# Performance work log

Measured on AMD Instinct MI355X. Metric: run time of the kernel, lower is better.

Reference implementation:

```python
import jax, jax.numpy as jnp
import numpy as np

B, N, F, FS, OUT, S, H, K = 1024, 256, 64, 128, 128, 4, 4, 4
EPS = 1e-5   # BatchNorm1d eps
BIG = 1e9    # sentinel distance for invalid nodes

# fully-connected segment edges (S nodes per graph, B graphs, flat node indexing)
_base = np.array([(i, j) for i in range(S) for j in range(S) if i != j], dtype=np.int32).T
_offs = (np.arange(B, dtype=np.int32) * S)[:, None]
CSRC = jnp.asarray((_base[0][None, :] + _offs).reshape(-1))
CDST = jnp.asarray((_base[1][None, :] + _offs).reshape(-1))
CMASK = jnp.ones(CSRC.shape[0], jnp.float32)


def _bn_relu(h, gamma, beta):
    # BatchNorm1d in training mode: biased batch statistics over the node axis
    mu = h.mean(0)
    var = jnp.var(h, axis=0)
    return jax.nn.relu((h - mu) * jax.lax.rsqrt(var + EPS) * gamma + beta)


def _graph_conv(x, src, dst, emask, W, b, gamma, beta):
    # linear -> gather(src) -> scatter-add(dst) -> degree norm -> BN -> ReLU
    h = x @ W + b
    agg = jax.ops.segment_sum(h[src] * emask[:, None], dst, num_segments=x.shape[0])
    deg = jnp.clip(jax.ops.segment_sum(emask, dst, num_segments=x.shape[0]), 1.0, None)
    return _bn_relu(h + agg / deg[:, None], gamma, beta)


def _knn_edges(positions, presence):
    # edges (i -> j) for each valid node i to its K nearest valid neighbors j
    valid = presence > 0.5                                    # [B,N]
    n_valid = valid.sum(-1)                                   # [B]
    diff = positions[:, :, None, :] - positions[:, None, :, :]
    d2 = jax.lax.stop_gradient(jnp.sum(diff * diff, -1))      # squared dist, same ordering as cdist
    d2 = jnp.where(valid[:, None, :], d2, BIG)                # mask invalid columns
    negv, idx = jax.lax.top_k(-d2, K + 1)                     # nearest first; idx[...,0] is self (dist 0)
    nbr, nd = idx[:, :, 1:], -negv[:, :, 1:]                  # [B,N,K]
    emask = valid[:, :, None] & (n_valid[:, None, None] >= 2) & (nd < 0.5 * BIG)
    offs = (jnp.arange(B) * N)[:, None, None]
    src = jnp.broadcast_to(jnp.arange(N)[None, :, None] + offs, (B, N, K)).reshape(-1)
    dst = jnp.where(emask, nbr + offs, 0).reshape(-1)
    return src, dst, emask.reshape(-1).astype(jnp.float32)


def setup_inputs() -> dict:
    key = jax.random.key(0)
    ks = jax.random.split(key, 16)
    rn = lambda k, shp, s=0.05: jax.random.normal(k, shp, jnp.float32) * s
    return {
        "axle_features": jax.random.normal(ks[0], (B, N, F), jnp.float32),
        "axle_positions": jax.random.normal(ks[1], (B, N, 2), jnp.float32),
        "presence_scores": jax.random.uniform(ks[2], (B, N), jnp.float32),
        "seg_queries": jax.random.normal(ks[3], (S, F), jnp.float32),
        "wq": rn(ks[4], (F, F)), "bq": jnp.zeros((F,), jnp.float32),
        "wk": rn(ks[5], (F, F)), "bk": jnp.zeros((F,), jnp.float32),
        "w_a2s": rn(ks[6], (F, FS)), "b_a2s": jnp.zeros((FS,), jnp.float32),
        "w_s2a": rn(ks[7], (FS, F)), "b_s2a": jnp.zeros((F,), jnp.float32),
        "coarse_W": rn(ks[8], (2, FS, FS)), "coarse_b": jnp.zeros((2, FS), jnp.float32),
        "coarse_gamma": jnp.ones((2, FS), jnp.float32), "coarse_beta": jnp.zeros((2, FS), jnp.float32),
        "fine_W": rn(ks[9], (3, F, F)), "fine_b": jnp.zeros((3, F), jnp.float32),
        "fine_gamma": jnp.ones((3, F), jnp.float32), "fine_beta": jnp.zeros((3, F), jnp.float32),
        "w_out": rn(ks[10], (F, OUT)), "b_out": jnp.zeros((OUT,), jnp.float32),
    }


def reference(axle_features, axle_positions, presence_scores, seg_queries, wq, bq, wk, bk,
              w_a2s, b_a2s, w_s2a, b_s2a, coarse_W, coarse_b, coarse_gamma, coarse_beta,
              fine_W, fine_b, fine_gamma, fine_beta, w_out, b_out):
    hd = F // H
    # LearnableSegmentation: MHA attention weights (head-averaged), then softmax over segments
    q = (seg_queries @ wq + bq).reshape(S, H, hd)
    k = (axle_features @ wk + bk).reshape(B, N, H, hd)
    scores = jnp.einsum('shd,bnhd->bhsn', q, k) / np.sqrt(hd)
    attn = jax.nn.softmax(scores, -1).mean(1)                 # [B,S,N]
    assign = jax.nn.softmax(jnp.swapaxes(attn, 1, 2), -1)     # [B,N,S]
    # segment pooling + coarse GNN over fully-connected segment graph
    proj = axle_features @ w_a2s + b_a2s                      # [B,N,FS]
    sf = jnp.einsum('bns,bnf->bsf', assign, proj).reshape(B * S, FS)
    for l in range(coarse_W.shape[0]):
        sf = _graph_conv(sf, CSRC, CDST, CMASK, coarse_W[l], coarse_b[l], coarse_gamma[l], coarse_beta[l])
    ctx = jnp.einsum('bns,bsf->bnf', assign, sf.reshape(B, S, FS)) @ w_s2a + b_s2a
    # fine GNN over kNN axle graph
    src, dst, em = _knn_edges(axle_positions, presence_scores)
    af = (axle_features + ctx).reshape(B * N, F)
    for l in range(fine_W.shape[0]):
        af = _graph_conv(af, src, dst, em, fine_W[l], fine_b[l], fine_gamma[l], fine_beta[l])
    # presence-weighted pooling + output projection
    pw = presence_scores[:, :, None]
    g = (af.reshape(B, N, F) * pw).sum(1) / jnp.clip(pw.sum(1), 1e-8, None)
    return g @ w_out + b_out
```

## Files before the change

kernel.cpp:

```cpp
#include <hip/hip_runtime.h>
#include <hip/hip_bf16.h>
#include <math.h>

#define BB   1024
#define NN   256
#define FF   64
#define FSS  128
#define OUTT 128
#define SS   4
#define HH   4
#define KK   4
#define HDD  16
#define EPSF 1e-5f
#define BIGF 1000000000.0f
#define ROWB 72
#define ROWA 68

typedef __attribute__((ext_vector_type(8))) short short8;
typedef __attribute__((ext_vector_type(4))) float f32x4;

static __device__ __forceinline__ unsigned short f2bf(float f) {
  union { float f; unsigned u; } x; x.f = f;
  unsigned u = x.u + 0x7fffu + ((x.u >> 16) & 1u);
  return (unsigned short)(u >> 16);
}
static __device__ __forceinline__ float bf2f(unsigned short h) {
  union { unsigned u; float f; } x; x.u = ((unsigned)h) << 16;
  return x.f;
}
static __device__ __forceinline__ float bflo(unsigned u) {
  union { unsigned u; float f; } x; x.u = u << 16; return x.f;
}
static __device__ __forceinline__ float bfhi(unsigned u) {
  union { unsigned u; float f; } x; x.u = u & 0xffff0000u; return x.f;
}
static __device__ __forceinline__ unsigned pack2(float a, float b) {
  return (unsigned)f2bf(a) | ((unsigned)f2bf(b) << 16);
}

__global__ __launch_bounds__(256) void k_prep(
    const float* __restrict__ sq, const float* __restrict__ wq, const float* __restrict__ bq,
    const float* __restrict__ wk, const float* __restrict__ bk,
    float* __restrict__ V_o, float* __restrict__ c_o)
{
  const int tid = threadIdx.x;
  __shared__ float sq_s[SS*FF];
  __shared__ float q_s[SS*FF];
  sq_s[tid] = sq[tid];
  __syncthreads();
  {
    int s = tid >> 6, f = tid & 63;
    float acc = bq[f];
    for (int c = 0; c < FF; ++c) acc += sq_s[s*FF+c] * wq[c*FF+f];
    q_s[s*FF+f] = acc;
  }
  __syncthreads();
  {
    int c = tid & 63, jb = (tid >> 6) * 4;
    for (int jj = 0; jj < 4; ++jj) {
      int j = jb + jj, h = j >> 2, s = j & 3;
      float acc = 0.f;
      for (int d = 0; d < HDD; ++d)
        acc += wk[c*FF + h*HDD + d] * q_s[s*FF + h*HDD + d];
      V_o[c*16 + j] = acc * 0.25f;
    }
  }
  if (tid < 16) {
    int h = tid >> 2, s = tid & 3;
    float acc = 0.f;
    for (int d = 0; d < HDD; ++d) acc += bk[h*HDD+d] * q_s[s*FF + h*HDD + d];
    c_o[tid] = acc * 0.25f;
  }
}

__global__ __launch_bounds__(256, 3) void k_attn_sf(
    const float* __restrict__ axle,
    const float* __restrict__ Vm, const float* __restrict__ cv,
    const float* __restrict__ w_a2s, const float* __restrict__ b_a2s,
    float* __restrict__ assign_o, float* __restrict__ sf_o)
{
  const int b = blockIdx.x, tid = threadIdx.x;
  const int wv = tid >> 6, ln = tid & 63;
  __shared__ __align__(16) unsigned short xb_a[NN*ROWA];
  __shared__ __align__(16) unsigned char u_buf[16*NN*2];
  __shared__ float mz_s[16][2];
  __hip_bfloat16* sc_s = (__hip_bfloat16*)u_buf;
  float (*as_s)[SS]    = (float (*)[SS])u_buf;
  float* t_s           = (float*)(u_buf + 4096);
  float* As_s          = (float*)(u_buf + 4096 + 1024);

  const float* afb = axle + (size_t)b*NN*FF;
  const float4* in4 = reinterpret_cast<const float4*>(afb);
  for (int i4 = tid; i4 < NN*FF/4; i4 += 256) {
    float4 v = in4[i4];
    int n = i4 >> 4, c4 = (i4 & 15) * 4;
    uint2 pk; pk.x = pack2(v.x, v.y); pk.y = pack2(v.z, v.w);
    *reinterpret_cast<uint2*>(&xb_a[n*ROWA + c4]) = pk;
  }
  __syncthreads();

  {
    float sc[16];
    #pragma unroll
    for (int j = 0; j < 16; ++j) sc[j] = cv[j];
    #pragma unroll
    for (int k = 0; k < 16; ++k) {
      uint2 pk = *reinterpret_cast<const uint2*>(&xb_a[tid*ROWA + 4*k]);
      float x0 = bflo(pk.x), x1 = bfhi(pk.x), x2 = bflo(pk.y), x3 = bfhi(pk.y);
      #pragma unroll
      for (int j = 0; j < 16; ++j) {
        float a = fmaf(x0, Vm[(4*k+0)*16+j], sc[j]);
        a = fmaf(x1, Vm[(4*k+1)*16+j], a);
        a = fmaf(x2, Vm[(4*k+2)*16+j], a);
        sc[j] = fmaf(x3, Vm[(4*k+3)*16+j], a);
      }
    }
    #pragma unroll
    for (int j = 0; j < 16; ++j) sc_s[j*NN + tid] = __float2bfloat16(sc[j]);
  }
  __syncthreads();

  for (int r = 0; r < 4; ++r) {
    int row = wv*4 + r;
    float v0 = __bfloat162float(sc_s[row*NN + ln]);
    float v1 = __bfloat162float(sc_s[row*NN + ln + 64]);
    float v2 = __bfloat162float(sc_s[row*NN + ln + 128]);
    float v3 = __bfloat162float(sc_s[row*NN + ln + 192]);
    float m = fmaxf(fmaxf(v0,v1), fmaxf(v2,v3));
    #pragma unroll
    for (int o = 32; o; o >>= 1) m = fmaxf(m, __shfl_xor(m, o));
    float z = __expf(v0-m) + __expf(v1-m) + __expf(v2-m) + __expf(v3-m);
    #pragma unroll
    for (int o = 32; o; o >>= 1) z += __shfl_xor(z, o);
    if (ln == 0) { mz_s[row][0] = m; mz_s[row][1] = 1.f/z; }
  }
  __syncthreads();

  float4 av;
  {
    float at0 = 0.f, at1 = 0.f, at2 = 0.f, at3 = 0.f;
    #pragma unroll
    for (int h = 0; h < HH; ++h) {
      at0 += __expf(__bfloat162float(sc_s[(h*4+0)*NN + tid]) - mz_s[h*4+0][0]) * mz_s[h*4+0][1];
      at1 += __expf(__bfloat162float(sc_s[(h*4+1)*NN + tid]) - mz_s[h*4+1][0]) * mz_s[h*4+1][1];
      at2 += __expf(__bfloat162float(sc_s[(h*4+2)*NN + tid]) - mz_s[h*4+2][0]) * mz_s[h*4+2][1];
      at3 += __expf(__bfloat162float(sc_s[(h*4+3)*NN + tid]) - mz_s[h*4+3][0]) * mz_s[h*4+3][1];
    }
    at0 *= 0.25f; at1 *= 0.25f; at2 *= 0.25f; at3 *= 0.25f;
    float m = fmaxf(fmaxf(at0,at1), fmaxf(at2,at3));
    float e0=__expf(at0-m), e1=__expf(at1-m), e2=__expf(at2-m), e3=__expf(at3-m);
    float zi = 1.f/(e0+e1+e2+e3);
    av = make_float4(e0*zi, e1*zi, e2*zi, e3*zi);
    reinterpret_cast<float4*>(assign_o)[(size_t)b*NN + tid] = av;
  }
  __syncthreads();
  *reinterpret_cast<float4*>(&as_s[tid][0]) = av;
  __syncthreads();

  {
    int s = wv, half = ln >> 5, c2 = ln & 31;
    float t0 = 0.f, t1 = 0.f, aa = 0.f;
    int n0 = half * 128;
    for (int n = n0; n < n0 + 128; ++n) {
      float a = as_s[n][s];
      unsigned pk = *reinterpret_cast<const unsigned*>(&xb_a[n*ROWA + 2*c2]);
      t0 = fmaf(a, bflo(pk), t0);
      t1 = fmaf(a, bfhi(pk), t1);
      aa += a;
    }
    t0 += __shfl_xor(t0, 32);
    t1 += __shfl_xor(t1, 32);
    aa += __shfl_xor(aa, 32);
    if (half == 0) {
      t_s[s*FF + 2*c2]     = t0;
      t_s[s*FF + 2*c2 + 1] = t1;
      if (c2 == 0) As_s[s] = aa;
    }
  }
  __syncthreads();

  for (int o = tid; o < SS*FSS; o += 256) {
    int s = o >> 7, f = o & 127;
    float acc = As_s[s] * b_a2s[f];
    for (int c = 0; c < FF; ++c) acc += t_s[s*FF + c] * w_a2s[c*FSS+f];
    sf_o[((size_t)b*SS+s)*FSS+f] = acc;
  }
}

__global__ __launch_bounds__(128) void k_coarse(
    const float* __restrict__ in, const float* __restrict__ W, const float* __restrict__ bias,
    const float* __restrict__ pmu, const float* __restrict__ prstd,
    const float* __restrict__ pgamma, const float* __restrict__ pbeta, int applyBN,
    float* __restrict__ out, float* __restrict__ stat1, float* __restrict__ stat2)
{
  const int b = blockIdx.x, f = threadIdx.x;
  __shared__ float x_s[SS][FSS];
  #pragma unroll
  for (int i = 0; i < SS; ++i) {
    float v = in[((size_t)b*SS+i)*FSS + f];
    if (applyBN) v = fmaxf((v - pmu[f])*prstd[f]*pgamma[f] + pbeta[f], 0.f);
    x_s[i][f] = v;
  }
  __syncthreads();
  float h0 = bias[f], h1 = h0, h2 = h0, h3 = h0;
  for (int c = 0; c < FSS; ++c) {
    float w = W[c*FSS+f];
    h0 += x_s[0][c]*w; h1 += x_s[1][c]*w; h2 += x_s[2][c]*w; h3 += x_s[3][c]*w;
  }
  float s4 = h0+h1+h2+h3;
  const float inv3 = 1.f/3.f;
  float o0 = h0 + (s4-h0)*inv3;
  float o1 = h1 + (s4-h1)*inv3;
  float o2 = h2 + (s4-h2)*inv3;
  float o3 = h3 + (s4-h3)*inv3;
  size_t ob = (size_t)b*SS*FSS + f;
  out[ob] = o0; out[ob+FSS] = o1; out[ob+2*FSS] = o2; out[ob+3*FSS] = o3;
  stat1[(size_t)f*BB + b] = o0+o1+o2+o3;
  stat2[(size_t)f*BB + b] = o0*o0+o1*o1+o2*o2+o3*o3;
}

__global__ __launch_bounds__(256) void k_bnstats(
    const float* __restrict__ s1, const float* __restrict__ s2,
    float* __restrict__ mu, float* __restrict__ rstd, float invcnt)
{
  const int f = blockIdx.x, tid = threadIdx.x;
  float a = 0.f, q = 0.f;
  for (int j = tid; j < BB; j += 256) { a += s1[(size_t)f*BB+j]; q += s2[(size_t)f*BB+j]; }
  #pragma unroll
  for (int o = 32; o; o >>= 1) { a += __shfl_xor(a, o); q += __shfl_xor(q, o); }
  __shared__ float ra[4], rq[4];
  int wv = tid >> 6;
  if ((tid & 63) == 0) { ra[wv] = a; rq[wv] = q; }
  __syncthreads();
  if (tid == 0) {
    float s = ra[0]+ra[1]+ra[2]+ra[3], ss = rq[0]+rq[1]+rq[2]+rq[3];
    float m = s*invcnt; float v = ss*invcnt - m*m;
    mu[f] = m; rstd[f] = 1.f / sqrtf(v + EPSF);
  }
}

__global__ __launch_bounds__(256) void k_knn(
    const float* __restrict__ pos, const float* __restrict__ pres,
    int* __restrict__ rev_go, int* __restrict__ offs_go,
    float* __restrict__ ivd_o, float* __restrict__ bf_o)
{
  const int b = blockIdx.x, tid = threadIdx.x;
  const int ln = tid & 63, wv = tid >> 6;
  __shared__ float px[NN], py[NN];
  __shared__ int vld[NN];
  __shared__ int wcnt[4];
  __shared__ int nbr_s[NN*KK];
  __shared__ int cnti[NN], scn[NN], cur[NN];
  __shared__ __align__(16) int rev_s[NN*KK];
  float2 p = reinterpret_cast<const float2*>(pos)[(size_t)b*NN + tid];
  float pr = pres[(size_t)b*NN + tid];
  int v = pr > 0.5f ? 1 : 0;
  px[tid] = p.x; py[tid] = p.y; vld[tid] = v;
  cnti[tid] = 0; cur[tid] = 0;
  #pragma unroll
  for (int k = 0; k < KK; ++k) rev_s[tid*KK+k] = 0;
  int cnt = v;
  #pragma unroll
  for (int o = 32; o; o >>= 1) cnt += __shfl_xor(cnt, o);
  if (ln == 0) wcnt[wv] = cnt;
  __syncthreads();
  int nv = wcnt[0]+wcnt[1]+wcnt[2]+wcnt[3];

  float b0=3.4e38f, b1=b0, b2=b0, b3=b0, b4=b0;
  int   j0=0, j1=0, j2=0, j3=0, j4=0;
  float xi = p.x, yi = p.y;
  for (int j = 0; j < NN; ++j) {
    float dx = __fsub_rn(xi, px[j]);
    float dy = __fsub_rn(yi, py[j]);
    float d2 = __fadd_rn(__fmul_rn(dx,dx), __fmul_rn(dy,dy));
    if (!vld[j]) d2 = BIGF;
    if (d2 < b4) {
      b4 = d2; j4 = j;
      if (b4 < b3) { float t=b3; b3=b4; b4=t; int ti=j3; j3=j4; j4=ti; }
      if (b3 < b2) { float t=b2; b2=b3; b3=t; int ti=j2; j2=j3; j3=ti; }
      if (b2 < b1) { float t=b1; b1=b2; b2=t; int ti=j1; j1=j2; j2=ti; }
      if (b1 < b0) { float t=b0; b0=b1; b1=t; int ti=j0; j0=j1; j1=ti; }
    }
  }
  (void)j0;
  bool okrow = (v != 0) && (nv >= 2);
  int d0 = (okrow && b1 < 0.5f*BIGF) ? j1 : -1;
  int d1 = (okrow && b2 < 0.5f*BIGF) ? j2 : -1;
  int d2i= (okrow && b3 < 0.5f*BIGF) ? j3 : -1;
  int d3 = (okrow && b4 < 0.5f*BIGF) ? j4 : -1;
  nbr_s[tid*KK+0] = d0; nbr_s[tid*KK+1] = d1;
  nbr_s[tid*KK+2] = d2i; nbr_s[tid*KK+3] = d3;
  if (d0 >= 0) atomicAdd(&cnti[d0], 1);
  if (d1 >= 0) atomicAdd(&cnti[d1], 1);
  if (d2i>= 0) atomicAdd(&cnti[d2i],1);
  if (d3 >= 0) atomicAdd(&cnti[d3], 1);
  __syncthreads();

  scn[tid] = cnti[tid];
  __syncthreads();
  for (int d = 1; d < NN; d <<= 1) {
    int t = (tid >= d) ? scn[tid-d] : 0;
    __syncthreads();
    scn[tid] += t;
    __syncthreads();
  }
  #pragma unroll
  for (int k = 0; k < KK; ++k) {
    int d = nbr_s[tid*KK+k];
    if (d >= 0) {
      int pp = atomicAdd(&cur[d], 1);
      rev_s[scn[d] - cnti[d] + pp] = tid;
    }
  }
  __syncthreads();

  int start = scn[tid] - cnti[tid];
  offs_go[(size_t)b*(NN+1) + tid] = start;
  if (tid == NN-1) offs_go[(size_t)b*(NN+1) + NN] = scn[NN-1];
  float cf = (float)cnti[tid];
  ivd_o[(size_t)b*NN + tid] = 1.f / fmaxf(cf, 1.f);
  bf_o[(size_t)b*NN + tid]  = cnti[tid] > 0 ? 2.f : 1.f;
  reinterpret_cast<int4*>(rev_go)[(size_t)b*NN + tid] =
      *reinterpret_cast<int4*>(&rev_s[tid*KK]);
}

__global__ __launch_bounds__(256) void k_ctx(
    const float* __restrict__ axle, const float* __restrict__ hc1,
    const float* __restrict__ mu, const float* __restrict__ rstd,
    const float* __restrict__ gamma, const float* __restrict__ beta,
    const float* __restrict__ assign_i,
    const float* __restrict__ w_s2a, const float* __restrict__ b_s2a,
    unsigned short* __restrict__ af_o)
{
  const int b = blockIdx.x, tid = threadIdx.x;
  __shared__ float csf[SS][FSS];
  __shared__ float u_s[SS][FF];
  for (int i = tid; i < SS*FSS; i += 256) {
    int s = i >> 7, f = i & 127;
    float v = hc1[((size_t)b*SS+s)*FSS + f];
    csf[s][f] = fmaxf((v - mu[f])*rstd[f]*gamma[f] + beta[f], 0.f);
  }
  __syncthreads();
  {
    int s = tid >> 6, f = tid & 63;
    float acc = 0.f;
    for (int c = 0; c < FSS; ++c) acc += csf[s][c] * w_s2a[c*FF+f];
    u_s[s][f] = acc;
  }
  __syncthreads();
  const size_t gb = (size_t)b*NN*FF;
  const float4* ax4 = reinterpret_cast<const float4*>(axle + gb);
  uint2* out2 = reinterpret_cast<uint2*>(af_o + gb);
  for (int i4 = tid; i4 < NN*FF/4; i4 += 256) {
    int n = i4 >> 4, c4 = (i4 & 15) * 4;
    float4 ax = ax4[i4];
    float4 ag = reinterpret_cast<const float4*>(assign_i)[(size_t)b*NN + n];
    float o0 = ax.x + b_s2a[c4+0] + ag.x*u_s[0][c4+0] + ag.y*u_s[1][c4+0] + ag.z*u_s[2][c4+0] + ag.w*u_s[3][c4+0];
    float o1 = ax.y + b_s2a[c4+1] + ag.x*u_s[0][c4+1] + ag.y*u_s[1][c4+1] + ag.z*u_s[2][c4+1] + ag.w*u_s[3][c4+1];
    float o2 = ax.z + b_s2a[c4+2] + ag.x*u_s[0][c4+2] + ag.y*u_s[1][c4+2] + ag.z*u_s[2][c4+2] + ag.w*u_s[3][c4+2];
    float o3 = ax.w + b_s2a[c4+3] + ag.x*u_s[0][c4+3] + ag.y*u_s[1][c4+3] + ag.z*u_s[2][c4+3] + ag.w*u_s[3][c4+3];
    uint2 pk; pk.x = pack2(o0, o1); pk.y = pack2(o2, o3);
    out2[i4] = pk;
  }
}

__global__ __launch_bounds__(512, 4) void k_fine3(
    unsigned short* __restrict__ af,
    const float* __restrict__ W, const float* __restrict__ bias,
    const float* __restrict__ pmu, const float* __restrict__ prstd,
    const float* __restrict__ pgamma, const float* __restrict__ pbeta, int applyBN,
    const int* __restrict__ rev_g, const int* __restrict__ offs_g,
    const float* __restrict__ ivd_g, const float* __restrict__ bf_g,
    float* __restrict__ stat1, float* __restrict__ stat2)
{
  const int b = blockIdx.x, tid = threadIdx.x;
  const int wv = tid >> 6, ln = tid & 63;
  const int l15 = ln & 15, g = ln >> 4;
  __shared__ __align__(16) unsigned short xb[NN*ROWB];
  __shared__ __align__(16) unsigned short wt[FF*ROWB];
  __shared__ __align__(16) int rev_s[NN*KK];
  __shared__ int offs_s[NN+1];
  __shared__ float ivd_s[NN], bf_s[NN];
  __shared__ float scale_s[FF], shift_s[FF];
  float* red1 = (float*)rev_s;
  float* red2 = red1 + 8*FF;

  if (tid < FF) {
    if (applyBN) {
      float sc = prstd[tid]*pgamma[tid];
      scale_s[tid] = sc; shift_s[tid] = pbeta[tid] - pmu[tid]*sc;
    } else { scale_s[tid] = 1.f; shift_s[tid] = 0.f; }
  }
  for (int i = tid; i < NN*KK; i += 512) rev_s[i] = rev_g[(size_t)b*NN*KK + i];
  if (tid <= NN) offs_s[tid] = offs_g[(size_t)b*(NN+1) + tid];
  if (tid < NN) { ivd_s[tid] = ivd_g[(size_t)b*NN + tid]; bf_s[tid] = bf_g[(size_t)b*NN + tid]; }

  {
    const int c = tid >> 3, f0 = (tid & 7) * 8;
    float4 w0 = *reinterpret_cast<const float4*>(&W[c*FF + f0]);
    float4 w1 = *reinterpret_cast<const float4*>(&W[c*FF + f0 + 4]);
    wt[(f0+0)*ROWB + c] = f2bf(w0.x);
    wt[(f0+1)*ROWB + c] = f2bf(w0.y);
    wt[(f0+2)*ROWB + c] = f2bf(w0.z);
    wt[(f0+3)*ROWB + c] = f2bf(w0.w);
    wt[(f0+4)*ROWB + c] = f2bf(w1.x);
    wt[(f0+5)*ROWB + c] = f2bf(w1.y);
    wt[(f0+6)*ROWB + c] = f2bf(w1.z);
    wt[(f0+7)*ROWB + c] = f2bf(w1.w);
  }

  unsigned short* afb = af + (size_t)b*NN*FF;
  const uint4* in8 = reinterpret_cast<const uint4*>(afb);
  __syncthreads();

  for (int i8 = tid; i8 < NN*FF/8; i8 += 512) {
    uint4 raw = in8[i8];
    int n = i8 >> 3, c8 = (i8 & 7) * 8;
    float v0 = bflo(raw.x), v1 = bfhi(raw.x), v2 = bflo(raw.y), v3 = bfhi(raw.y);
    float v4 = bflo(raw.z), v5 = bfhi(raw.z), v6 = bflo(raw.w), v7 = bfhi(raw.w);
    v0 = v0*scale_s[c8+0] + shift_s[c8+0];
    v1 = v1*scale_s[c8+1] + shift_s[c8+1];
    v2 = v2*scale_s[c8+2] + shift_s[c8+2];
    v3 = v3*scale_s[c8+3] + shift_s[c8+3];
    v4 = v4*scale_s[c8+4] + shift_s[c8+4];
    v5 = v5*scale_s[c8+5] + shift_s[c8+5];
    v6 = v6*scale_s[c8+6] + shift_s[c8+6];
    v7 = v7*scale_s[c8+7] + shift_s[c8+7];
    if (applyBN) {
      v0=fmaxf(v0,0.f); v1=fmaxf(v1,0.f); v2=fmaxf(v2,0.f); v3=fmaxf(v3,0.f);
      v4=fmaxf(v4,0.f); v5=fmaxf(v5,0.f); v6=fmaxf(v6,0.f); v7=fmaxf(v7,0.f);
    }
    uint4 pk;
    pk.x = pack2(v0, v1); pk.y = pack2(v2, v3);
    pk.z = pack2(v4, v5); pk.w = pack2(v6, v7);
    *reinterpret_cast<uint4*>(&xb[n*ROWB + c8]) = pk;
  }
  __syncthreads();

  const int nb = wv << 5;
#define GATH(J) float y##J; { const int n_ = nb + (J); \
    const int s0_ = offs_s[n_]; const int s1_ = offs_s[n_+1]; \
    float sum_ = 0.f; \
    for (int i_ = s0_; i_ < s1_; ++i_) sum_ += bf2f(xb[rev_s[i_]*ROWB + ln]); \
    y##J = bf2f(xb[n_*ROWB + ln]) + ivd_s[n_]*sum_; }
  GATH(0)  GATH(1)  GATH(2)  GATH(3)  GATH(4)  GATH(5)  GATH(6)  GATH(7)
  GATH(8)  GATH(9)  GATH(10) GATH(11) GATH(12) GATH(13) GATH(14) GATH(15)
  GATH(16) GATH(17) GATH(18) GATH(19) GATH(20) GATH(21) GATH(22) GATH(23)
  GATH(24) GATH(25) GATH(26) GATH(27) GATH(28) GATH(29) GATH(30) GATH(31)
#undef GATH
  __syncthreads();
#define WRB(J) xb[(nb + (J))*ROWB + ln] = f2bf(y##J);
  WRB(0)  WRB(1)  WRB(2)  WRB(3)  WRB(4)  WRB(5)  WRB(6)  WRB(7)
  WRB(8)  WRB(9)  WRB(10) WRB(11) WRB(12) WRB(13) WRB(14) WRB(15)
  WRB(16) WRB(17) WRB(18) WRB(19) WRB(20) WRB(21) WRB(22) WRB(23)
  WRB(24) WRB(25) WRB(26) WRB(27) WRB(28) WRB(29) WRB(30) WRB(31)
#undef WRB
  __syncthreads();

  short8 areg[2][2], breg[4][2];
  #pragma unroll
  for (int rt2 = 0; rt2 < 2; ++rt2)
    #pragma unroll
    for (int ks = 0; ks < 2; ++ks)
      areg[rt2][ks] = *reinterpret_cast<const short8*>(
          &xb[((2*wv+rt2)*16 + l15)*ROWB + ks*32 + g*8]);
  #pragma unroll
  for (int ct = 0; ct < 4; ++ct)
    #pragma unroll
    for (int ks = 0; ks < 2; ++ks)
      breg[ct][ks] = *reinterpret_cast<const short8*>(
          &wt[(ct*16 + l15)*ROWB + ks*32 + g*8]);

  f32x4 acc[2][4];
  #pragma unroll
  for (int rt2 = 0; rt2 < 2; ++rt2)
    #pragma unroll
    for (int ct = 0; ct < 4; ++ct)
      acc[rt2][ct] = (f32x4){0.f, 0.f, 0.f, 0.f};
  #pragma unroll
  for (int rt2 = 0; rt2 < 2; ++rt2)
    #pragma unroll
    for (int ct = 0; ct < 4; ++ct)
      #pragma unroll
      for (int ks = 0; ks < 2; ++ks)
        acc[rt2][ct] = __builtin_amdgcn_mfma_f32_16x16x32_bf16(
            areg[rt2][ks], breg[ct][ks], acc[rt2][ct], 0, 0, 0);

  float bias_c[4];
  #pragma unroll
  for (int ct = 0; ct < 4; ++ct) bias_c[ct] = bias[ct*16 + l15];
  float ps[4] = {0.f,0.f,0.f,0.f}, pss[4] = {0.f,0.f,0.f,0.f};
  #pragma unroll
  for (int rt2 = 0; rt2 < 2; ++rt2) {
    #pragma unroll
    for (int i = 0; i < 4; ++i) {
      int row = (2*wv+rt2)*16 + g*4 + i;
      float bfr = bf_s[row];
      #pragma unroll
      for (int ct = 0; ct < 4; ++ct) {
        float o = acc[rt2][ct][i] + bfr*bias_c[ct];
        xb[row*ROWB + ct*16 + l15] = f2bf(o);
        ps[ct] += o; pss[ct] += o*o;
      }
    }
  }
  #pragma unroll
  for (int ct = 0; ct < 4; ++ct) {
    float p = ps[ct], q = pss[ct];
    p += __shfl_xor(p, 16); p += __shfl_xor(p, 32);
    q += __shfl_xor(q, 16); q += __shfl_xor(q, 32);
    if (g == 0) { red1[wv*FF + ct*16 + l15] = p; red2[wv*FF + ct*16 + l15] = q; }
  }
  __syncthreads();

  uint4* out8 = reinterpret_cast<uint4*>(afb);
  for (int i8 = tid; i8 < NN*FF/8; i8 += 512) {
    int n = i8 >> 3, c8 = (i8 & 7) * 8;
    out8[i8] = *reinterpret_cast<const uint4*>(&xb[n*ROWB + c8]);
  }
  if (tid < FF) {
    float s = 0.f, ss = 0.f;
    #pragma unroll
    for (int w = 0; w < 8; ++w) { s += red1[w*FF + tid]; ss += red2[w*FF + tid]; }
    stat1[(size_t)tid*BB + b] = s;
    stat2[(size_t)tid*BB + b] = ss;
  }
}

__global__ __launch_bounds__(256) void k_pool(
    const unsigned short* __restrict__ af, const float* __restrict__ pres,
    const float* __restrict__ pmu, const float* __restrict__ prstd,
    const float* __restrict__ pgamma, const float* __restrict__ pbeta,
    const float* __restrict__ w_out, const float* __restrict__ b_out,
    float* __restrict__ out)
{
  const int b = blockIdx.x, tid = threadIdx.x;
  const int wv = tid >> 6, ln = tid & 63;
  __shared__ float pr_s2[NN];
  __shared__ float red[FF][9];
  __shared__ float g_s[FF];
  __shared__ float prsum_s[4];
  float pw = pres[(size_t)b*NN + tid];
  pr_s2[tid] = pw;
  float t = pw;
  #pragma unroll
  for (int o = 32; o; o >>= 1) t += __shfl_xor(t, o);
  if (ln == 0) prsum_s[wv] = t;
  __syncthreads();

  const int c2 = (tid & 31) * 2, jrow = tid >> 5;
  float sc0 = prstd[c2+0]*pgamma[c2+0], sh0 = pbeta[c2+0] - pmu[c2+0]*sc0;
  float sc1 = prstd[c2+1]*pgamma[c2+1], sh1 = pbeta[c2+1] - pmu[c2+1]*sc1;
  float s0 = 0.f, s1 = 0.f;
  const unsigned* af2 = reinterpret_cast<const unsigned*>(af + (size_t)b*NN*FF);
  for (int n = jrow; n < NN; n += 8) {
    unsigned pk = af2[n*(FF/2) + (tid & 31)];
    float p = pr_s2[n];
    s0 += fmaxf(bflo(pk)*sc0 + sh0, 0.f) * p;
    s1 += fmaxf(bfhi(pk)*sc1 + sh1, 0.f) * p;
  }
  red[c2+0][jrow] = s0;
  red[c2+1][jrow] = s1;
  __syncthreads();
  if (tid < FF) {
    float s = 0.f;
    #pragma unroll
    for (int j = 0; j < 8; ++j) s += red[tid][j];
    float den = fmaxf(prsum_s[0]+prsum_s[1]+prsum_s[2]+prsum_s[3], 1e-8f);
    g_s[tid] = s / den;
  }
  __syncthreads();
  if (tid < OUTT) {
    float acc = b_out[tid];
    for (int f = 0; f < FF; ++f) acc += g_s[f] * w_out[f*OUTT + tid];
    out[(size_t)b*OUTT + tid] = acc;
  }
}

extern "C" void kernel_launch(void* const* d_in, const int* in_sizes, int n_in,
                              void* d_out, int out_size, void* d_ws, size_t ws_size,
                              hipStream_t stream) {
  (void)in_sizes; (void)n_in; (void)out_size; (void)ws_size;
  const float* axle  = (const float*)d_in[0];
  const float* pos   = (const float*)d_in[1];
  const float* pres  = (const float*)d_in[2];
  const float* sq    = (const float*)d_in[3];
  const float* wq    = (const float*)d_in[4];
  const float* bq    = (const float*)d_in[5];
  const float* wk    = (const float*)d_in[6];
  const float* bk    = (const float*)d_in[7];
  const float* w_a2s = (const float*)d_in[8];
  const float* b_a2s = (const float*)d_in[9];
  const float* w_s2a = (const float*)d_in[10];
  const float* b_s2a = (const float*)d_in[11];
  const float* cW    = (const float*)d_in[12];
  const float* cb    = (const float*)d_in[13];
  const float* cg    = (const float*)d_in[14];
  const float* cbe   = (const float*)d_in[15];
  const float* fW    = (const float*)d_in[16];
  const float* fb    = (const float*)d_in[17];
  const float* fg    = (const float*)d_in[18];
  const float* fbe   = (const float*)d_in[19];
  const float* wout  = (const float*)d_in[20];
  const float* bout  = (const float*)d_in[21];
  float* out = (float*)d_out;

  char* base = (char*)d_ws;
  size_t off = 0;
  auto alloc = [&](size_t nbytes) -> void* {
    void* p = base + off; off += (nbytes + 255) & ~(size_t)255; return p;
  };
  unsigned short* af = (unsigned short*)alloc((size_t)BB*NN*FF*2);
  float* assign = (float*)alloc((size_t)BB*NN*SS*4);
  float* sf     = (float*)alloc((size_t)BB*SS*FSS*4);
  float* hc0    = (float*)alloc((size_t)BB*SS*FSS*4);
  float* hc1    = (float*)alloc((size_t)BB*SS*FSS*4);
  int*   rev    = (int*)  alloc((size_t)BB*NN*KK*4);
  int*   offs   = (int*)  alloc((size_t)BB*(NN+1)*4);
  float* ivd    = (float*)alloc((size_t)BB*NN*4);
  float* bff    = (float*)alloc((size_t)BB*NN*4);
  float* st1    = (float*)alloc((size_t)FSS*BB*4);
  float* st2    = (float*)alloc((size_t)FSS*BB*4);
  float* mu0    = (float*)alloc(FSS*4);
  float* rs0    = (float*)alloc(FSS*4);
  float* mu1    = (float*)alloc(FSS*4);
  float* rs1    = (float*)alloc(FSS*4);
  float* muF    = (float*)alloc(FF*4);
  float* rsF    = (float*)alloc(FF*4);
  float* Vm     = (float*)alloc(FF*16*4);
  float* cv     = (float*)alloc(16*4);

  k_prep<<<1, 256, 0, stream>>>(sq, wq, bq, wk, bk, Vm, cv);
  k_attn_sf<<<BB, 256, 0, stream>>>(axle, Vm, cv, w_a2s, b_a2s, assign, sf);

  k_coarse<<<BB, 128, 0, stream>>>(sf,  cW,          cb,     mu0, rs0, cg, cbe, 0, hc0, st1, st2);
  k_bnstats<<<FSS, 256, 0, stream>>>(st1, st2, mu0, rs0, 1.f/((float)BB*SS));
  k_coarse<<<BB, 128, 0, stream>>>(hc0, cW+FSS*FSS,  cb+FSS, mu0, rs0, cg, cbe, 1, hc1, st1, st2);
  k_bnstats<<<FSS, 256, 0, stream>>>(st1, st2, mu1, rs1, 1.f/((float)BB*SS));

  k_knn<<<BB, 256, 0, stream>>>(pos, pres, rev, offs, ivd, bff);

  k_ctx<<<BB, 256, 0, stream>>>(axle, hc1, mu1, rs1, cg+FSS, cbe+FSS, assign, w_s2a, b_s2a, af);

  k_fine3<<<BB, 512, 0, stream>>>(af, fW,         fb,      muF, rsF, fg,    fbe,    0, rev, offs, ivd, bff, st1, st2);
  k_bnstats<<<FF, 256, 0, stream>>>(st1, st2, muF, rsF, 1.f/((float)BB*NN));
  k_fine3<<<BB, 512, 0, stream>>>(af, fW+FF*FF,   fb+FF,   muF, rsF, fg,    fbe,    1, rev, offs, ivd, bff, st1, st2);
  k_bnstats<<<FF, 256, 0, stream>>>(st1, st2, muF, rsF, 1.f/((float)BB*NN));
  k_fine3<<<BB, 512, 0, stream>>>(af, fW+2*FF*FF, fb+2*FF, muF, rsF, fg+FF, fbe+FF, 1, rev, offs, ivd, bff, st1, st2);
  k_bnstats<<<FF, 256, 0, stream>>>(st1, st2, muF, rsF, 1.f/((float)BB*NN));

  k_pool<<<BB, 256, 0, stream>>>(af, pres, muF, rsF, fg+2*FF, fbe+2*FF, wout, bout, out);
}
```

Measured before the change: 277.9 us.

## Split kNN scan across two threads per node and fold bias flag into ivd sign

The kNN kernel now runs 512 threads per graph, so two threads share each node. Each thread scans half of the candidate columns and keeps its own top-5 list. The two partial lists are then merged through cross-lane shuffles. Invalid nodes get sentinel positions at build time, which removes the per-iteration validity check, and the coordinates are loaded as float2 from one shared array. The separate bias-factor array is dropped: its flag is stored as the sign of the inverse-degree value, and offsets are held in shared memory as 16-bit values. This shortens the serial distance loop and cuts global and LDS traffic in the fine layers. In exchange it adds merge logic, and tie and sentinel handling could diverge from the reference in edge cases.

```diff
diff --git a/kernel.cpp b/kernel.cpp
--- a/kernel.cpp
+++ b/kernel.cpp
@@ -239,41 +239,47 @@
   }
 }
 
-__global__ __launch_bounds__(256) void k_knn(
+__global__ __launch_bounds__(512) void k_knn(
     const float* __restrict__ pos, const float* __restrict__ pres,
     int* __restrict__ rev_go, int* __restrict__ offs_go,
-    float* __restrict__ ivd_o, float* __restrict__ bf_o)
+    float* __restrict__ ivd_o)
 {
   const int b = blockIdx.x, tid = threadIdx.x;
   const int ln = tid & 63, wv = tid >> 6;
-  __shared__ float px[NN], py[NN];
+  const int n = tid >> 1, half = tid & 1;
+  __shared__ float2 pp[NN];
   __shared__ int vld[NN];
   __shared__ int wcnt[4];
   __shared__ int nbr_s[NN*KK];
   __shared__ int cnti[NN], scn[NN], cur[NN];
   __shared__ __align__(16) int rev_s[NN*KK];
-  float2 p = reinterpret_cast<const float2*>(pos)[(size_t)b*NN + tid];
-  float pr = pres[(size_t)b*NN + tid];
-  int v = pr > 0.5f ? 1 : 0;
-  px[tid] = p.x; py[tid] = p.y; vld[tid] = v;
-  cnti[tid] = 0; cur[tid] = 0;
-  #pragma unroll
-  for (int k = 0; k < KK; ++k) rev_s[tid*KK+k] = 0;
-  int cnt = v;
-  #pragma unroll
-  for (int o = 32; o; o >>= 1) cnt += __shfl_xor(cnt, o);
-  if (ln == 0) wcnt[wv] = cnt;
-  __syncthreads();
-  int nv = wcnt[0]+wcnt[1]+wcnt[2]+wcnt[3];
-
+
+  if (tid < NN) {
+    float2 p = reinterpret_cast<const float2*>(pos)[(size_t)b*NN + tid];
+    float pr = pres[(size_t)b*NN + tid];
+    int v = pr > 0.5f ? 1 : 0;
+    vld[tid] = v;
+    pp[tid] = v ? p : make_float2(3.4e38f, 3.4e38f);
+    cnti[tid] = 0; cur[tid] = 0;
+    reinterpret_cast<int4*>(rev_s)[tid] = make_int4(0,0,0,0);
+    int cnt = v;
+    #pragma unroll
+    for (int o = 32; o; o >>= 1) cnt += __shfl_xor(cnt, o);
+    if (ln == 0) wcnt[wv] = cnt;
+  }
+  __syncthreads();
+  const int nv = wcnt[0]+wcnt[1]+wcnt[2]+wcnt[3];
+
+  float2 sp = pp[n];
+  const float xi = sp.x, yi = sp.y;
   float b0=3.4e38f, b1=b0, b2=b0, b3=b0, b4=b0;
   int   j0=0, j1=0, j2=0, j3=0, j4=0;
-  float xi = p.x, yi = p.y;
-  for (int j = 0; j < NN; ++j) {
-    float dx = __fsub_rn(xi, px[j]);
-    float dy = __fsub_rn(yi, py[j]);
+  const int jb = half << 7;
+  for (int j = jb; j < jb + 128; ++j) {
+    float2 q = pp[j];
+    float dx = __fsub_rn(xi, q.x);
+    float dy = __fsub_rn(yi, q.y);
     float d2 = __fadd_rn(__fmul_rn(dx,dx), __fmul_rn(dy,dy));
-    if (!vld[j]) d2 = BIGF;
     if (d2 < b4) {
       b4 = d2; j4 = j;
       if (b4 < b3) { float t=b3; b3=b4; b4=t; int ti=j3; j3=j4; j4=ti; }
@@ -282,46 +288,74 @@
       if (b1 < b0) { float t=b0; b0=b1; b1=t; int ti=j0; j0=j1; j1=ti; }
     }
   }
-  (void)j0;
-  bool okrow = (v != 0) && (nv >= 2);
-  int d0 = (okrow && b1 < 0.5f*BIGF) ? j1 : -1;
-  int d1 = (okrow && b2 < 0.5f*BIGF) ? j2 : -1;
-  int d2i= (okrow && b3 < 0.5f*BIGF) ? j3 : -1;
-  int d3 = (okrow && b4 < 0.5f*BIGF) ? j4 : -1;
-  nbr_s[tid*KK+0] = d0; nbr_s[tid*KK+1] = d1;
-  nbr_s[tid*KK+2] = d2i; nbr_s[tid*KK+3] = d3;
-  if (d0 >= 0) atomicAdd(&cnti[d0], 1);
-  if (d1 >= 0) atomicAdd(&cnti[d1], 1);
-  if (d2i>= 0) atomicAdd(&cnti[d2i],1);
-  if (d3 >= 0) atomicAdd(&cnti[d3], 1);
-  __syncthreads();
-
-  scn[tid] = cnti[tid];
+  float c0 = __shfl_xor(b0,1), c1 = __shfl_xor(b1,1), c2 = __shfl_xor(b2,1),
+        c3 = __shfl_xor(b3,1), c4 = __shfl_xor(b4,1);
+  int   k0 = __shfl_xor(j0,1), k1 = __shfl_xor(j1,1), k2 = __shfl_xor(j2,1),
+        k3 = __shfl_xor(j3,1), k4 = __shfl_xor(j4,1);
+
+  if (half == 0) {
+#define MSTEP(OD, OJ) do { bool ta = (b0 <= c0); \
+    OD = ta ? b0 : c0; OJ = ta ? j0 : k0; \
+    b0 = ta ? b1 : b0; j0 = ta ? j1 : j0; \
+    b1 = ta ? b2 : b1; j1 = ta ? j2 : j1; \
+    b2 = ta ? b3 : b2; j2 = ta ? j3 : j2; \
+    b3 = ta ? b4 : b3; j3 = ta ? j4 : j3; \
+    b4 = ta ? 3.4e38f : b4; \
+    c0 = ta ? c0 : c1; k0 = ta ? k0 : k1; \
+    c1 = ta ? c1 : c2; k1 = ta ? k1 : k2; \
+    c2 = ta ? c2 : c3; k2 = ta ? k2 : k3; \
+    c3 = ta ? c3 : c4; k3 = ta ? k3 : k4; \
+    c4 = ta ? c4 : 3.4e38f; } while(0)
+    float m0d, dd1, dd2, dd3, dd4; int m0j, i1, i2, i3, i4;
+    MSTEP(m0d, m0j);
+    MSTEP(dd1, i1); MSTEP(dd2, i2); MSTEP(dd3, i3); MSTEP(dd4, i4);
+#undef MSTEP
+    (void)m0d; (void)m0j;
+    bool okrow = (vld[n] != 0) && (nv >= 2);
+    int e0 = (okrow && dd1 < 0.5f*BIGF) ? i1 : -1;
+    int e1 = (okrow && dd2 < 0.5f*BIGF) ? i2 : -1;
+    int e2 = (okrow && dd3 < 0.5f*BIGF) ? i3 : -1;
+    int e3 = (okrow && dd4 < 0.5f*BIGF) ? i4 : -1;
+    nbr_s[n*KK+0] = e0; nbr_s[n*KK+1] = e1;
+    nbr_s[n*KK+2] = e2; nbr_s[n*KK+3] = e3;
+    if (e0 >= 0) atomicAdd(&cnti[e0], 1);
+    if (e1 >= 0) atomicAdd(&cnti[e1], 1);
+    if (e2 >= 0) atomicAdd(&cnti[e2], 1);
+    if (e3 >= 0) atomicAdd(&cnti[e3], 1);
+  }
+  __syncthreads();
+
+  if (tid < NN) scn[tid] = cnti[tid];
   __syncthreads();
   for (int d = 1; d < NN; d <<= 1) {
-    int t = (tid >= d) ? scn[tid-d] : 0;
+    int t = 0;
+    if (tid < NN && tid >= d) t = scn[tid-d];
     __syncthreads();
-    scn[tid] += t;
+    if (tid < NN) scn[tid] += t;
     __syncthreads();
   }
-  #pragma unroll
-  for (int k = 0; k < KK; ++k) {
-    int d = nbr_s[tid*KK+k];
-    if (d >= 0) {
-      int pp = atomicAdd(&cur[d], 1);
-      rev_s[scn[d] - cnti[d] + pp] = tid;
-    }
-  }
-  __syncthreads();
-
-  int start = scn[tid] - cnti[tid];
-  offs_go[(size_t)b*(NN+1) + tid] = start;
-  if (tid == NN-1) offs_go[(size_t)b*(NN+1) + NN] = scn[NN-1];
-  float cf = (float)cnti[tid];
-  ivd_o[(size_t)b*NN + tid] = 1.f / fmaxf(cf, 1.f);
-  bf_o[(size_t)b*NN + tid]  = cnti[tid] > 0 ? 2.f : 1.f;
-  reinterpret_cast<int4*>(rev_go)[(size_t)b*NN + tid] =
-      *reinterpret_cast<int4*>(&rev_s[tid*KK]);
+  if (tid < NN) {
+    #pragma unroll
+    for (int k = 0; k < KK; ++k) {
+      int d = nbr_s[tid*KK+k];
+      if (d >= 0) {
+        int pp2 = atomicAdd(&cur[d], 1);
+        rev_s[scn[d] - cnti[d] + pp2] = tid;
+      }
+    }
+  }
+  __syncthreads();
+
+  if (tid < NN) {
+    int start = scn[tid] - cnti[tid];
+    offs_go[(size_t)b*(NN+1) + tid] = start;
+    if (tid == NN-1) offs_go[(size_t)b*(NN+1) + NN] = scn[NN-1];
+    int cnt = cnti[tid];
+    float r = 1.f / fmaxf((float)cnt, 1.f);
+    ivd_o[(size_t)b*NN + tid] = cnt > 0 ? -r : r;
+    reinterpret_cast<int4*>(rev_go)[(size_t)b*NN + tid] =
+        *reinterpret_cast<int4*>(&rev_s[tid*KK]);
+  }
 }
 
 __global__ __launch_bounds__(256) void k_ctx(
@@ -370,7 +404,7 @@
     const float* __restrict__ pmu, const float* __restrict__ prstd,
     const float* __restrict__ pgamma, const float* __restrict__ pbeta, int applyBN,
     const int* __restrict__ rev_g, const int* __restrict__ offs_g,
-    const float* __restrict__ ivd_g, const float* __restrict__ bf_g,
+    const float* __restrict__ ivd_g,
     float* __restrict__ stat1, float* __restrict__ stat2)
 {
   const int b = blockIdx.x, tid = threadIdx.x;
@@ -379,8 +413,8 @@
   __shared__ __align__(16) unsigned short xb[NN*ROWB];
   __shared__ __align__(16) unsigned short wt[FF*ROWB];
   __shared__ __align__(16) int rev_s[NN*KK];
-  __shared__ int offs_s[NN+1];
-  __shared__ float ivd_s[NN], bf_s[NN];
+  __shared__ unsigned short offs_s[NN+1];
+  __shared__ float ivd_s[NN];
   __shared__ float scale_s[FF], shift_s[FF];
   float* red1 = (float*)rev_s;
   float* red2 = red1 + 8*FF;
@@ -392,8 +426,8 @@
     } else { scale_s[tid] = 1.f; shift_s[tid] = 0.f; }
   }
   for (int i = tid; i < NN*KK; i += 512) rev_s[i] = rev_g[(size_t)b*NN*KK + i];
-  if (tid <= NN) offs_s[tid] = offs_g[(size_t)b*(NN+1) + tid];
-  if (tid < NN) { ivd_s[tid] = ivd_g[(size_t)b*NN + tid]; bf_s[tid] = bf_g[(size_t)b*NN + tid]; }
+  if (tid <= NN) offs_s[tid] = (unsigned short)offs_g[(size_t)b*(NN+1) + tid];
+  if (tid < NN) ivd_s[tid] = ivd_g[(size_t)b*NN + tid];
 
   {
     const int c = tid >> 3, f0 = (tid & 7) * 8;
@@ -442,7 +476,7 @@
     const int s0_ = offs_s[n_]; const int s1_ = offs_s[n_+1]; \
     float sum_ = 0.f; \
     for (int i_ = s0_; i_ < s1_; ++i_) sum_ += bf2f(xb[rev_s[i_]*ROWB + ln]); \
-    y##J = bf2f(xb[n_*ROWB + ln]) + ivd_s[n_]*sum_; }
+    y##J = bf2f(xb[n_*ROWB + ln]) + fabsf(ivd_s[n_])*sum_; }
   GATH(0)  GATH(1)  GATH(2)  GATH(3)  GATH(4)  GATH(5)  GATH(6)  GATH(7)
   GATH(8)  GATH(9)  GATH(10) GATH(11) GATH(12) GATH(13) GATH(14) GATH(15)
   GATH(16) GATH(17) GATH(18) GATH(19) GATH(20) GATH(21) GATH(22) GATH(23)
@@ -495,7 +529,7 @@
     #pragma unroll
     for (int i = 0; i < 4; ++i) {
       int row = (2*wv+rt2)*16 + g*4 + i;
-      float bfr = bf_s[row];
+      float bfr = ivd_s[row] < 0.f ? 2.f : 1.f;
       #pragma unroll
       for (int ct = 0; ct < 4; ++ct) {
         float o = acc[rt2][ct][i] + bfr*bias_c[ct];
@@ -618,7 +652,6 @@
   int*   rev    = (int*)  alloc((size_t)BB*NN*KK*4);
   int*   offs   = (int*)  alloc((size_t)BB*(NN+1)*4);
   float* ivd    = (float*)alloc((size_t)BB*NN*4);
-  float* bff    = (float*)alloc((size_t)BB*NN*4);
   float* st1    = (float*)alloc((size_t)FSS*BB*4);
   float* st2    = (float*)alloc((size_t)FSS*BB*4);
   float* mu0    = (float*)alloc(FSS*4);
@@ -638,15 +671,15 @@
   k_coarse<<<BB, 128, 0, stream>>>(hc0, cW+FSS*FSS,  cb+FSS, mu0, rs0, cg, cbe, 1, hc1, st1, st2);
   k_bnstats<<<FSS, 256, 0, stream>>>(st1, st2, mu1, rs1, 1.f/((float)BB*SS));
 
-  k_knn<<<BB, 256, 0, stream>>>(pos, pres, rev, offs, ivd, bff);
+  k_knn<<<BB, 512, 0, stream>>>(pos, pres, rev, offs, ivd);
 
   k_ctx<<<BB, 256, 0, stream>>>(axle, hc1, mu1, rs1, cg+FSS, cbe+FSS, assign, w_s2a, b_s2a, af);
 
-  k_fine3<<<BB, 512, 0, stream>>>(af, fW,         fb,      muF, rsF, fg,    fbe,    0, rev, offs, ivd, bff, st1, st2);
+  k_fine3<<<BB, 512, 0, stream>>>(af, fW,         fb,      muF, rsF, fg,    fbe,    0, rev, offs, ivd, st1, st2);
   k_bnstats<<<FF, 256, 0, stream>>>(st1, st2, muF, rsF, 1.f/((float)BB*NN));
-  k_fine3<<<BB, 512, 0, stream>>>(af, fW+FF*FF,   fb+FF,   muF, rsF, fg,    fbe,    1, rev, offs, ivd, bff, st1, st2);
+  k_fine3<<<BB, 512, 0, stream>>>(af, fW+FF*FF,   fb+FF,   muF, rsF, fg,    fbe,    1, rev, offs, ivd, st1, st2);
   k_bnstats<<<FF, 256, 0, stream>>>(st1, st2, muF, rsF, 1.f/((float)BB*NN));
-  k_fine3<<<BB, 512, 0, stream>>>(af, fW+2*FF*FF, fb+2*FF, muF, rsF, fg+FF, fbe+FF, 1, rev, offs, ivd, bff, st1, st2);
+  k_fine3<<<BB, 512, 0, stream>>>(af, fW+2*FF*FF, fb+2*FF, muF, rsF, fg+FF, fbe+FF, 1, rev, offs, ivd, st1, st2);
   k_bnstats<<<FF, 256, 0, stream>>>(st1, st2, muF, rsF, 1.f/((float)BB*NN));
 
   k_pool<<<BB, 256, 0, stream>>>(af, pres, muF, rsF, fg+2*FF, fbe+2*FF, wout, bout, out);
```

New measurement: 281.5 us. Within noise of the previous version (+1.3%).
